# Kernel tuning notes

Hardware: AMD Instinct MI355X
Metric: run time of the kernel (lower is better)

## Reference

```python
import jax, jax.numpy as jnp
import numpy as np
import math

B, S, HID = 2, 2048, 4096
NH, NKV, HD = 32, 8, 128
ROPE_BASE = 10000.0


def _rope_tables(b, s, hd):
    inv_freq = 1.0 / (ROPE_BASE ** (jnp.arange(0, hd, 2, dtype=jnp.float32) / hd))
    t = jnp.arange(s, dtype=jnp.float32)
    freqs = jnp.outer(t, inv_freq)            # [s, hd/2]
    emb = jnp.concatenate([freqs, freqs], -1)  # [s, hd]
    cos = jnp.broadcast_to(jnp.cos(emb)[None], (b, s, hd))
    sin = jnp.broadcast_to(jnp.sin(emb)[None], (b, s, hd))
    return cos, sin


def setup_inputs() -> dict:
    key = jax.random.key(0)
    ks = jax.random.split(key, 5)
    hidden_states = jax.random.normal(ks[0], (B, S, HID), dtype=jnp.float32)
    # additive causal mask [B,1,S,S]: 0 on/below diagonal, large negative above
    causal = jnp.tril(jnp.ones((S, S), dtype=bool))
    attention_mask = jnp.where(causal, 0.0, jnp.finfo(jnp.float32).min)[None, None]
    attention_mask = jnp.broadcast_to(attention_mask, (B, 1, S, S)).astype(jnp.float32)
    cos, sin = _rope_tables(B, S, HD)
    sc = 0.02
    Wq = jax.random.normal(ks[1], (NH * HD, HID), dtype=jnp.float32) * sc
    Wk = jax.random.normal(ks[2], (NKV * HD, HID), dtype=jnp.float32) * sc
    Wv = jax.random.normal(ks[3], (NKV * HD, HID), dtype=jnp.float32) * sc
    Wo = jax.random.normal(ks[4], (HID, NH * HD), dtype=jnp.float32) * sc
    return {"hidden_states": hidden_states, "attention_mask": attention_mask,
            "cos": cos, "sin": sin, "Wq": Wq, "Wk": Wk, "Wv": Wv, "Wo": Wo}


def _rotate_half(x):
    x1, x2 = jnp.split(x, 2, axis=-1)
    return jnp.concatenate([-x2, x1], axis=-1)


def reference(hidden_states, attention_mask, cos, sin, Wq, Wk, Wv, Wo):
    b, s, _ = hidden_states.shape
    # projections (nn.Linear: x @ W.T, no bias)
    q = jnp.einsum('bsh,oh->bso', hidden_states, Wq).reshape(b, s, NH, HD).transpose(0, 2, 1, 3)
    k = jnp.einsum('bsh,oh->bso', hidden_states, Wk).reshape(b, s, NKV, HD).transpose(0, 2, 1, 3)
    v = jnp.einsum('bsh,oh->bso', hidden_states, Wv).reshape(b, s, NKV, HD).transpose(0, 2, 1, 3)
    # RoPE (cos/sin: [b,s,hd] -> unsqueeze head dim)
    c, sn = cos[:, None], sin[:, None]
    q = q * c + _rotate_half(q) * sn
    k = k * c + _rotate_half(k) * sn
    # repeat_kv: [b,nkv,s,d] -> [b,nh,s,d] (repeat_interleave over head dim)
    n_rep = NH // NKV
    k = jnp.repeat(k, n_rep, axis=1)
    v = jnp.repeat(v, n_rep, axis=1)
    # eager attention
    scores = jnp.einsum('bhqd,bhkd->bhqk', q, k) / math.sqrt(HD)
    scores = scores + attention_mask[:, :, :, :k.shape[2]]
    probs = jax.nn.softmax(scores.astype(jnp.float32), axis=-1).astype(q.dtype)
    attn = jnp.einsum('bhqk,bhkd->bhqd', probs, v)
    attn = attn.transpose(0, 2, 1, 3).reshape(b, s, NH * HD)
    return jnp.einsum('bso,ho->bsh', attn, Wo)
```

## Files before the change

### kernel.cpp

```cpp
#include <hip/hip_runtime.h>
#include <hip/hip_bf16.h>
#include <cstdint>

#define S_LEN 2048
#define HIDDEN 4096
#define NH 32
#define NKV 8
#define HD 128
#define BATCH 2
#define MROWS (BATCH * S_LEN)

typedef float f32x4 __attribute__((ext_vector_type(4)));
typedef __bf16 bf16x8 __attribute__((ext_vector_type(8)));
typedef __bf16 bf16x4 __attribute__((ext_vector_type(4)));

static __device__ inline f32x4 mfma16(bf16x8 a, bf16x8 b, f32x4 c) {
    return __builtin_amdgcn_mfma_f32_16x16x32_bf16(a, b, c, 0, 0, 0);
}

static __device__ inline void gl_lds16(const __bf16* g, __bf16* l) {
    __builtin_amdgcn_global_load_lds(
        (const __attribute__((address_space(1))) void*)g,
        (__attribute__((address_space(3))) void*)l, 16, 0, 0);
}

#define LGKM0()  asm volatile("s_waitcnt lgkmcnt(0)" ::: "memory")
#define SCHEDB() __builtin_amdgcn_sched_barrier(0)
#define SBAR()   __builtin_amdgcn_s_barrier()

__global__ __launch_bounds__(256) void conv_f32_bf16(const float* __restrict__ in,
                                                     __bf16* __restrict__ out, int n8) {
    int i = blockIdx.x * 256 + threadIdx.x;
    if (i >= n8) return;
    const float4* p = (const float4*)in + (size_t)i * 2;
    float4 a = p[0], b = p[1];
    bf16x8 v;
    v[0] = (__bf16)a.x; v[1] = (__bf16)a.y; v[2] = (__bf16)a.z; v[3] = (__bf16)a.w;
    v[4] = (__bf16)b.x; v[5] = (__bf16)b.y; v[6] = (__bf16)b.z; v[7] = (__bf16)b.w;
    ((bf16x8*)out)[i] = v;
}

template<int MODE, int BM>
__global__ __launch_bounds__(512, 2) void gemm256(const __bf16* __restrict__ A,
                                                  const __bf16* __restrict__ B,
                                                  float* __restrict__ Cf,
                                                  __bf16* __restrict__ Qo,
                                                  __bf16* __restrict__ Ko,
                                                  __bf16* __restrict__ Vo,
                                                  int N, int K, int nbx) {
    constexpr int MF = BM / 32;
    constexpr int MH = BM / 64;
    __shared__ __bf16 As[2][BM * 64];
    __shared__ __bf16 Bs[2][256 * 64];
    const int tid = threadIdx.x, lane = tid & 63;
    const int lq = lane & 15, hi2 = lane >> 4;
    const int wv = tid >> 6;
    const int wr = wv >> 2, wc = wv & 3;

    const int cpx = gridDim.x >> 3;
    const int bid = blockIdx.x;
    const int swz = (bid & 7) * cpx + (bid >> 3);
    const int bx = swz % nbx, by = swz / nbx;
    const int brow = by * BM, bcol = bx * 256;

    f32x4 acc[MF][4] = {};
    bf16x8 af[MH][2], bfr[2][2];
    const int NT = K >> 6;

    auto stageA = [&](int bb, int kt, int roff) {
        #pragma unroll
        for (int r = 0; r < 2; ++r) {
            int i = r * 512 + tid;
            int row = i >> 3, sl = i & 7, lsl = sl ^ (row & 7);
            gl_lds16(A + (size_t)(brow + roff + row) * K + kt * 64 + lsl * 8,
                     &As[bb][roff * 64 + i * 8]);
        }
    };
    auto stageB = [&](int bb, int kt, int roff) {
        #pragma unroll
        for (int r = 0; r < 2; ++r) {
            int i = r * 512 + tid;
            int row = i >> 3, sl = i & 7, lsl = sl ^ (row & 7);
            gl_lds16(B + (size_t)(bcol + roff + row) * K + kt * 64 + lsl * 8,
                     &Bs[bb][roff * 64 + i * 8]);
        }
    };
    auto loadA = [&](int bb, int mq) {
        #pragma unroll
        for (int mi = 0; mi < MH; ++mi) {
            int row = wr * (BM / 2) + (mq * MH + mi) * 16 + lq;
            #pragma unroll
            for (int kk = 0; kk < 2; ++kk) {
                int lsl = (kk * 4 + hi2) ^ (row & 7);
                af[mi][kk] = *(const bf16x8*)&As[bb][row * 64 + lsl * 8];
            }
        }
    };
    auto loadB = [&](int bb, int nq) {
        #pragma unroll
        for (int ni = 0; ni < 2; ++ni) {
            int row = wc * 64 + (nq * 2 + ni) * 16 + lq;
            #pragma unroll
            for (int kk = 0; kk < 2; ++kk) {
                int lsl = (kk * 4 + hi2) ^ (row & 7);
                bfr[ni][kk] = *(const bf16x8*)&Bs[bb][row * 64 + lsl * 8];
            }
        }
    };
    auto mmaq = [&](int mq, int nq) {
        __builtin_amdgcn_s_setprio(1);
        #pragma unroll
        for (int kk = 0; kk < 2; ++kk)
            #pragma unroll
            for (int mi = 0; mi < MH; ++mi)
                #pragma unroll
                for (int ni = 0; ni < 2; ++ni)
                    acc[mq * MH + mi][nq * 2 + ni] =
                        mfma16(af[mi][kk], bfr[ni][kk], acc[mq * MH + mi][nq * 2 + ni]);
        __builtin_amdgcn_s_setprio(0);
    };

    stageA(0, 0, 0);
    if constexpr (BM == 256) stageA(0, 0, 128);
    stageB(0, 0, 0);
    stageB(0, 0, 128);

    for (int t = 0; t < NT; ++t) {
        const int cur = t & 1, nxt = cur ^ 1;
        const int tn = (t + 1 < NT) ? t + 1 : NT - 1;
        stageA(nxt, tn, 0);
        if constexpr (BM == 256) stageA(nxt, tn, 128);
        stageB(nxt, tn, 0);
        if constexpr (BM == 256) { asm volatile("s_waitcnt vmcnt(6)" ::: "memory"); }
        else                     { asm volatile("s_waitcnt vmcnt(4)" ::: "memory"); }
        SBAR(); SCHEDB();
        loadA(cur, 0); loadB(cur, 0);
        LGKM0(); SCHEDB();
        mmaq(0, 0);
        SBAR(); SCHEDB();
        loadB(cur, 1);
        stageB(nxt, tn, 128);
        SBAR(); SCHEDB();
        LGKM0(); SCHEDB();
        mmaq(0, 1);
        SBAR(); SCHEDB();
        loadA(cur, 1);
        SBAR(); SCHEDB();
        LGKM0(); SCHEDB();
        mmaq(1, 1);
        SBAR(); SCHEDB();
        loadB(cur, 0);
        SBAR(); SCHEDB();
        LGKM0(); SCHEDB();
        mmaq(1, 0);
        SBAR(); SCHEDB();
    }

    #pragma unroll
    for (int m = 0; m < MF; ++m) {
        #pragma unroll
        for (int n = 0; n < 4; ++n) {
            int row0 = brow + wr * (BM / 2) + m * 16 + (hi2 << 2);
            int col  = bcol + wc * 64 + n * 16 + lq;
            if constexpr (MODE == 3) {
                if (col < NKV * HD) {
                    #pragma unroll
                    for (int j = 0; j < 4; ++j)
                        Ko[(size_t)(row0 + j) * (NKV * HD) + col] = (__bf16)acc[m][n][j];
                } else {
                    int c2 = col - NKV * HD;
                    int hkv = c2 >> 7, d = c2 & (HD - 1);
                    int bb2 = row0 >> 11, s = row0 & (S_LEN - 1);
                    bf16x4 t4;
                    #pragma unroll
                    for (int j = 0; j < 4; ++j) t4[j] = (__bf16)acc[m][n][j];
                    *(bf16x4*)&Vo[((size_t)((bb2 * NKV + hkv) * HD + d)) * S_LEN + s] = t4;
                }
            } else if constexpr (MODE == 1) {
                #pragma unroll
                for (int j = 0; j < 4; ++j)
                    Cf[(size_t)(row0 + j) * N + col] = acc[m][n][j];
            } else {
                #pragma unroll
                for (int j = 0; j < 4; ++j)
                    Qo[(size_t)(row0 + j) * N + col] = (__bf16)acc[m][n][j];
            }
        }
    }
}

__global__ __launch_bounds__(256) void rope_kernel(__bf16* __restrict__ X,
                                                   const float* __restrict__ ct,
                                                   const float* __restrict__ st,
                                                   int nheads, int total) {
    int idx = blockIdx.x * 256 + threadIdx.x;
    if (idx >= total) return;
    int d  = idx & 63;
    int hh = (idx >> 6) % nheads;
    int m  = idx / (64 * nheads);
    __bf16* p = X + (size_t)m * (nheads * HD) + hh * HD;
    float c = ct[(size_t)m * HD + d];
    float s = st[(size_t)m * HD + d];
    float x1 = (float)p[d], x2 = (float)p[d + 64];
    p[d]      = (__bf16)(x1 * c - x2 * s);
    p[d + 64] = (__bf16)(x2 * c + x1 * s);
}

__global__ __launch_bounds__(256, 3) void attn_kernel(const __bf16* __restrict__ Q,
                                                      const __bf16* __restrict__ K,
                                                      const __bf16* __restrict__ V,
                                                      __bf16* __restrict__ O) {
    constexpr int QB = 128, KB = 32;
    constexpr int nqb = S_LEN / QB;
    const int bid = blockIdx.x;
    const int qb  = nqb - 1 - (bid % nqb);
    const int h   = (bid / nqb) % NH;
    const int b   = bid / (nqb * NH);
    const int hkv = h >> 2;
    const int tid = threadIdx.x, lane = tid & 63, w = tid >> 6;
    const int lq = lane & 15, hi2 = lane >> 4;
    const int q0 = qb * QB, qrow_lo = q0 + w * 32;

    __shared__ __bf16 Ks[2][KB * HD];
    __shared__ __bf16 Vt[2][HD * KB];
    __shared__ __bf16 Pl[4][2][16][40];

    bf16x8 qf[2][4];
    #pragma unroll
    for (int mt = 0; mt < 2; ++mt) {
        int row = qrow_lo + mt * 16 + lq;
        const __bf16* qp = Q + ((size_t)(b * S_LEN + row)) * (NH * HD) + h * HD + hi2 * 8;
        #pragma unroll
        for (int c = 0; c < 4; ++c) qf[mt][c] = *(const bf16x8*)(qp + c * 32);
    }

    f32x4 o_acc[2][8] = {};
    float m_r[2] = {-1e30f, -1e30f}, l_r[2] = {0.f, 0.f};
    const float scale = 0.08838834764831843f;
    const int nkb = (q0 + QB) / KB;

    auto stage = [&](int bb, int k0s) {
        #pragma unroll
        for (int r = 0; r < 2; ++r) {
            int i = r * 256 + tid;
            {   int row = i >> 4, sl = i & 15, lsl = sl ^ (row & 7);
                gl_lds16(&K[((size_t)(b * S_LEN + k0s + row)) * (NKV * HD) + hkv * HD + lsl * 8],
                         &Ks[bb][i * 8]); }
            {   int d = i >> 2, sl = i & 3, lsl = sl ^ (d & 3);
                gl_lds16(&V[((size_t)((b * NKV + hkv) * HD + d)) * S_LEN + k0s + lsl * 8],
                         &Vt[bb][i * 8]); }
        }
    };

    stage(0, 0);
    for (int kb = 0; kb < nkb; ++kb) {
        int kn = (kb + 1 < nkb) ? kb + 1 : kb;
        stage((kb + 1) & 1, kn * KB);
        asm volatile("s_waitcnt vmcnt(4)" ::: "memory");
        SBAR(); SCHEDB();
        const int cur = kb & 1;
        const int k0  = kb * KB;
        const __bf16* ks = &Ks[cur][0];
        const __bf16* vt = &Vt[cur][0];

        f32x4 sc[2][2] = {};
        #pragma unroll
        for (int t = 0; t < 2; ++t) {
            int krow = t * 16 + lq;
            #pragma unroll
            for (int c = 0; c < 4; ++c) {
                int psl = (c * 4 + hi2) ^ (krow & 7);
                bf16x8 kf = *(const bf16x8*)&ks[krow * HD + psl * 8];
                sc[0][t] = mfma16(kf, qf[0][c], sc[0][t]);
                sc[1][t] = mfma16(kf, qf[1][c], sc[1][t]);
            }
        }

        #pragma unroll
        for (int mt = 0; mt < 2; ++mt) {
            int q_abs = qrow_lo + mt * 16 + lq;
            #pragma unroll
            for (int t = 0; t < 2; ++t)
                #pragma unroll
                for (int j = 0; j < 4; ++j) {
                    int kv_abs = k0 + t * 16 + hi2 * 4 + j;
                    sc[mt][t][j] = (kv_abs > q_abs) ? -1e30f : sc[mt][t][j] * scale;
                }
            float pmax = fmaxf(
                fmaxf(fmaxf(sc[mt][0][0], sc[mt][0][1]), fmaxf(sc[mt][0][2], sc[mt][0][3])),
                fmaxf(fmaxf(sc[mt][1][0], sc[mt][1][1]), fmaxf(sc[mt][1][2], sc[mt][1][3])));
            pmax = fmaxf(pmax, __shfl_xor(pmax, 16));
            pmax = fmaxf(pmax, __shfl_xor(pmax, 32));
            float mn = fmaxf(m_r[mt], pmax);
            float sf = __expf(m_r[mt] - mn);
            m_r[mt] = mn;
            float rs = 0.f;
            #pragma unroll
            for (int t = 0; t < 2; ++t)
                #pragma unroll
                for (int j = 0; j < 4; ++j) {
                    float p = __expf(sc[mt][t][j] - mn);
                    sc[mt][t][j] = p;
                    rs += p;
                }
            rs += __shfl_xor(rs, 16);
            rs += __shfl_xor(rs, 32);
            l_r[mt] = l_r[mt] * sf + rs;
            #pragma unroll
            for (int dt = 0; dt < 8; ++dt)
                #pragma unroll
                for (int j = 0; j < 4; ++j) o_acc[mt][dt][j] *= sf;
            #pragma unroll
            for (int t = 0; t < 2; ++t) {
                bf16x4 pw;
                #pragma unroll
                for (int j = 0; j < 4; ++j) pw[j] = (__bf16)sc[mt][t][j];
                *(bf16x4*)&Pl[w][mt][lq][t * 16 + hi2 * 4] = pw;
            }
        }

        LGKM0(); SCHEDB();
        bf16x8 pf0 = *(const bf16x8*)&Pl[w][0][lq][hi2 * 8];
        bf16x8 pf1 = *(const bf16x8*)&Pl[w][1][lq][hi2 * 8];

        #pragma unroll
        for (int dt = 0; dt < 8; ++dt) {
            int vrow = dt * 16 + lq;
            int psl  = hi2 ^ (vrow & 3);
            bf16x8 vf = *(const bf16x8*)&vt[vrow * KB + psl * 8];
            o_acc[0][dt] = mfma16(vf, pf0, o_acc[0][dt]);
            o_acc[1][dt] = mfma16(vf, pf1, o_acc[1][dt]);
        }
        LGKM0(); SCHEDB();
        SBAR(); SCHEDB();
    }

    #pragma unroll
    for (int mt = 0; mt < 2; ++mt) {
        float inv = 1.0f / l_r[mt];
        int q_abs = qrow_lo + mt * 16 + lq;
        __bf16* op = O + ((size_t)(b * S_LEN + q_abs)) * (NH * HD) + h * HD;
        #pragma unroll
        for (int dt = 0; dt < 8; ++dt) {
            bf16x4 t4;
            #pragma unroll
            for (int j = 0; j < 4; ++j) t4[j] = (__bf16)(o_acc[mt][dt][j] * inv);
            *(bf16x4*)&op[dt * 16 + hi2 * 4] = t4;
        }
    }
}

extern "C" void kernel_launch(void* const* d_in, const int* in_sizes, int n_in,
                              void* d_out, int out_size, void* d_ws, size_t ws_size,
                              hipStream_t stream) {
    const float* X  = (const float*)d_in[0];
    const float* ct = (const float*)d_in[2];
    const float* st = (const float*)d_in[3];
    const float* Wq = (const float*)d_in[4];
    const float* Wk = (const float*)d_in[5];
    const float* Wv = (const float*)d_in[6];
    const float* Wo = (const float*)d_in[7];
    float* out = (float*)d_out;

    const size_t MEL  = (size_t)MROWS * HIDDEN;
    const size_t KVEL = (size_t)MROWS * (NKV * HD);
    const int NQKV = NH * HD + 2 * NKV * HD;

    __bf16* Wqkv = (__bf16*)d_ws;
    __bf16* Xb   = Wqkv + (size_t)NQKV * HIDDEN;
    __bf16* Qb   = Xb + MEL;
    __bf16* Kb   = Qb + MEL;
    __bf16* VtG  = Kb + KVEL;
    __bf16* Ab   = Wqkv;
    __bf16* Wob  = Xb;

    dim3 blk(256);
    hipLaunchKernelGGL(conv_f32_bf16, dim3((int)(MEL / 8 / 256)), blk, 0, stream, X,  Xb, (int)(MEL / 8));
    hipLaunchKernelGGL(conv_f32_bf16, dim3((int)(MEL / 8 / 256)), blk, 0, stream, Wq, Wqkv, (int)(MEL / 8));
    hipLaunchKernelGGL(conv_f32_bf16, dim3((int)(KVEL / 8 / 256)), blk, 0, stream,
                       Wk, Wqkv + (size_t)HIDDEN * HIDDEN, (int)(KVEL / 8));
    hipLaunchKernelGGL(conv_f32_bf16, dim3((int)(KVEL / 8 / 256)), blk, 0, stream,
                       Wv, Wqkv + (size_t)(HIDDEN + NKV * HD) * HIDDEN, (int)(KVEL / 8));

    hipLaunchKernelGGL((gemm256<0, 256>), dim3(256), dim3(512), 0, stream,
                       Xb, Wqkv, nullptr, Qb, nullptr, nullptr, NH * HD, HIDDEN, 16);
    hipLaunchKernelGGL((gemm256<3, 128>), dim3(256), dim3(512), 0, stream,
                       Xb, Wqkv + (size_t)HIDDEN * HIDDEN, nullptr, nullptr, Kb, VtG,
                       2 * NKV * HD, HIDDEN, 8);

    hipLaunchKernelGGL(rope_kernel, dim3((MROWS * NH * 64) / 256), blk, 0, stream,
                       Qb, ct, st, NH, MROWS * NH * 64);
    hipLaunchKernelGGL(rope_kernel, dim3((MROWS * NKV * 64) / 256), blk, 0, stream,
                       Kb, ct, st, NKV, MROWS * NKV * 64);

    hipLaunchKernelGGL(conv_f32_bf16, dim3((int)(MEL / 8 / 256)), blk, 0, stream, Wo, Wob, (int)(MEL / 8));

    hipLaunchKernelGGL(attn_kernel, dim3(BATCH * NH * (S_LEN / 128)), blk, 0, stream,
                       Qb, Kb, VtG, Ab);

    hipLaunchKernelGGL((gemm256<1, 256>), dim3(256), dim3(512), 0, stream,
                       Ab, Wob, out, nullptr, nullptr, nullptr, HIDDEN, HIDDEN, 16);
}
```

Baseline: 675.9 us.

## Pair causal query blocks per workgroup and use lazy exp2 softmax rescaling

Each attention workgroup now processes two complementary query blocks (a long one and a short one), so all 512 workgroups do equal causal work. The grid is remapped to spread workgroups across XCDs. The K/V prefetch pipeline runs continuously across both passes. Separately, the softmax scale and log2(e) are folded into Q, exp is replaced by exp2, masking runs only on diagonal tiles, and rescaling of the accumulator is skipped unless the running max grows by more than a threshold. Risks are higher register pressure from the loop nesting and slightly different numerics from folding the scale into bf16 Q.

```diff
diff --git a/kernel.cpp b/kernel.cpp
--- a/kernel.cpp
+++ b/kernel.cpp
@@ -212,32 +212,23 @@
                                                       __bf16* __restrict__ O) {
     constexpr int QB = 128, KB = 32;
     constexpr int nqb = S_LEN / QB;
-    const int bid = blockIdx.x;
-    const int qb  = nqb - 1 - (bid % nqb);
-    const int h   = (bid / nqb) % NH;
-    const int b   = bid / (nqb * NH);
+    const int cpx = gridDim.x >> 3;
+    const int b0 = blockIdx.x;
+    const int bid = (b0 & 7) * cpx + (b0 >> 3);
+    const int pair = bid & 7;
+    const int h    = (bid >> 3) & (NH - 1);
+    const int b    = bid >> 8;
     const int hkv = h >> 2;
     const int tid = threadIdx.x, lane = tid & 63, w = tid >> 6;
     const int lq = lane & 15, hi2 = lane >> 4;
-    const int q0 = qb * QB, qrow_lo = q0 + w * 32;
 
     __shared__ __bf16 Ks[2][KB * HD];
     __shared__ __bf16 Vt[2][HD * KB];
     __shared__ __bf16 Pl[4][2][16][40];
 
-    bf16x8 qf[2][4];
-    #pragma unroll
-    for (int mt = 0; mt < 2; ++mt) {
-        int row = qrow_lo + mt * 16 + lq;
-        const __bf16* qp = Q + ((size_t)(b * S_LEN + row)) * (NH * HD) + h * HD + hi2 * 8;
-        #pragma unroll
-        for (int c = 0; c < 4; ++c) qf[mt][c] = *(const bf16x8*)(qp + c * 32);
-    }
-
-    f32x4 o_acc[2][8] = {};
-    float m_r[2] = {-1e30f, -1e30f}, l_r[2] = {0.f, 0.f};
-    const float scale = 0.08838834764831843f;
-    const int nkb = (q0 + QB) / KB;
+    const int qbA = nqb - 1 - pair;
+    const int nkbA = 4 * (qbA + 1);
+    const int T = nkbA + 4 * (pair + 1);
 
     auto stage = [&](int bb, int k0s) {
         #pragma unroll
@@ -252,100 +243,134 @@
         }
     };
 
+    const float c2 = 0.08838834764831843f * 1.4426950408889634f;
+
     stage(0, 0);
-    for (int kb = 0; kb < nkb; ++kb) {
-        int kn = (kb + 1 < nkb) ? kb + 1 : kb;
-        stage((kb + 1) & 1, kn * KB);
-        asm volatile("s_waitcnt vmcnt(4)" ::: "memory");
-        SBAR(); SCHEDB();
-        const int cur = kb & 1;
-        const int k0  = kb * KB;
-        const __bf16* ks = &Ks[cur][0];
-        const __bf16* vt = &Vt[cur][0];
-
-        f32x4 sc[2][2] = {};
-        #pragma unroll
-        for (int t = 0; t < 2; ++t) {
-            int krow = t * 16 + lq;
+    int tt = 0;
+    #pragma unroll 1
+    for (int pass = 0; pass < 2; ++pass) {
+        const int qb = pass ? pair : qbA;
+        const int q0 = qb * QB, qrow_lo = q0 + w * 32;
+        const int nkb = 4 * (qb + 1);
+
+        bf16x8 qf[2][4];
+        #pragma unroll
+        for (int mt = 0; mt < 2; ++mt) {
+            int row = qrow_lo + mt * 16 + lq;
+            const __bf16* qp = Q + ((size_t)(b * S_LEN + row)) * (NH * HD) + h * HD + hi2 * 8;
             #pragma unroll
             for (int c = 0; c < 4; ++c) {
-                int psl = (c * 4 + hi2) ^ (krow & 7);
-                bf16x8 kf = *(const bf16x8*)&ks[krow * HD + psl * 8];
-                sc[0][t] = mfma16(kf, qf[0][c], sc[0][t]);
-                sc[1][t] = mfma16(kf, qf[1][c], sc[1][t]);
-            }
+                bf16x8 v = *(const bf16x8*)(qp + c * 32);
+                #pragma unroll
+                for (int e = 0; e < 8; ++e) v[e] = (__bf16)((float)v[e] * c2);
+                qf[mt][c] = v;
+            }
+        }
+
+        f32x4 o_acc[2][8] = {};
+        float m_r[2] = {-1e30f, -1e30f}, l_r[2] = {0.f, 0.f};
+
+        #pragma unroll 1
+        for (int kb = 0; kb < nkb; ++kb, ++tt) {
+            int tn = (tt + 1 < T) ? tt + 1 : T - 1;
+            int k0n = (tn < nkbA ? tn : tn - nkbA) * KB;
+            stage((tt + 1) & 1, k0n);
+            asm volatile("s_waitcnt vmcnt(4)" ::: "memory");
+            SBAR(); SCHEDB();
+            const int cur = tt & 1;
+            const int k0  = kb * KB;
+            const __bf16* ks = &Ks[cur][0];
+            const __bf16* vt = &Vt[cur][0];
+
+            f32x4 sc[2][2] = {};
+            #pragma unroll
+            for (int t = 0; t < 2; ++t) {
+                int krow = t * 16 + lq;
+                #pragma unroll
+                for (int c = 0; c < 4; ++c) {
+                    int psl = (c * 4 + hi2) ^ (krow & 7);
+                    bf16x8 kf = *(const bf16x8*)&ks[krow * HD + psl * 8];
+                    sc[0][t] = mfma16(kf, qf[0][c], sc[0][t]);
+                    sc[1][t] = mfma16(kf, qf[1][c], sc[1][t]);
+                }
+            }
+
+            #pragma unroll
+            for (int mt = 0; mt < 2; ++mt) {
+                int q_abs = qrow_lo + mt * 16 + lq;
+                if (k0 + KB - 1 > qrow_lo + mt * 16) {
+                    #pragma unroll
+                    for (int t = 0; t < 2; ++t)
+                        #pragma unroll
+                        for (int j = 0; j < 4; ++j) {
+                            int kv_abs = k0 + t * 16 + hi2 * 4 + j;
+                            if (kv_abs > q_abs) sc[mt][t][j] = -1e30f;
+                        }
+                }
+                float pmax = fmaxf(
+                    fmaxf(fmaxf(sc[mt][0][0], sc[mt][0][1]), fmaxf(sc[mt][0][2], sc[mt][0][3])),
+                    fmaxf(fmaxf(sc[mt][1][0], sc[mt][1][1]), fmaxf(sc[mt][1][2], sc[mt][1][3])));
+                pmax = fmaxf(pmax, __shfl_xor(pmax, 16));
+                pmax = fmaxf(pmax, __shfl_xor(pmax, 32));
+                if (!__all(pmax - m_r[mt] <= 8.0f)) {
+                    float mn = fmaxf(m_r[mt], pmax);
+                    float sf = __builtin_amdgcn_exp2f(m_r[mt] - mn);
+                    m_r[mt] = mn;
+                    l_r[mt] *= sf;
+                    #pragma unroll
+                    for (int dt = 0; dt < 8; ++dt)
+                        #pragma unroll
+                        for (int j = 0; j < 4; ++j) o_acc[mt][dt][j] *= sf;
+                }
+                float rs = 0.f;
+                #pragma unroll
+                for (int t = 0; t < 2; ++t)
+                    #pragma unroll
+                    for (int j = 0; j < 4; ++j) {
+                        float p = __builtin_amdgcn_exp2f(sc[mt][t][j] - m_r[mt]);
+                        sc[mt][t][j] = p;
+                        rs += p;
+                    }
+                rs += __shfl_xor(rs, 16);
+                rs += __shfl_xor(rs, 32);
+                l_r[mt] += rs;
+                #pragma unroll
+                for (int t = 0; t < 2; ++t) {
+                    bf16x4 pw;
+                    #pragma unroll
+                    for (int j = 0; j < 4; ++j) pw[j] = (__bf16)sc[mt][t][j];
+                    *(bf16x4*)&Pl[w][mt][lq][t * 16 + hi2 * 4] = pw;
+                }
+            }
+
+            LGKM0(); SCHEDB();
+            bf16x8 pf0 = *(const bf16x8*)&Pl[w][0][lq][hi2 * 8];
+            bf16x8 pf1 = *(const bf16x8*)&Pl[w][1][lq][hi2 * 8];
+
+            #pragma unroll
+            for (int dt = 0; dt < 8; ++dt) {
+                int vrow = dt * 16 + lq;
+                int psl  = hi2 ^ (vrow & 3);
+                bf16x8 vf = *(const bf16x8*)&vt[vrow * KB + psl * 8];
+                o_acc[0][dt] = mfma16(vf, pf0, o_acc[0][dt]);
+                o_acc[1][dt] = mfma16(vf, pf1, o_acc[1][dt]);
+            }
+            LGKM0(); SCHEDB();
+            SBAR(); SCHEDB();
         }
 
         #pragma unroll
         for (int mt = 0; mt < 2; ++mt) {
+            float inv = 1.0f / l_r[mt];
             int q_abs = qrow_lo + mt * 16 + lq;
-            #pragma unroll
-            for (int t = 0; t < 2; ++t)
-                #pragma unroll
-                for (int j = 0; j < 4; ++j) {
-                    int kv_abs = k0 + t * 16 + hi2 * 4 + j;
-                    sc[mt][t][j] = (kv_abs > q_abs) ? -1e30f : sc[mt][t][j] * scale;
-                }
-            float pmax = fmaxf(
-                fmaxf(fmaxf(sc[mt][0][0], sc[mt][0][1]), fmaxf(sc[mt][0][2], sc[mt][0][3])),
-                fmaxf(fmaxf(sc[mt][1][0], sc[mt][1][1]), fmaxf(sc[mt][1][2], sc[mt][1][3])));
-            pmax = fmaxf(pmax, __shfl_xor(pmax, 16));
-            pmax = fmaxf(pmax, __shfl_xor(pmax, 32));
-            float mn = fmaxf(m_r[mt], pmax);
-            float sf = __expf(m_r[mt] - mn);
-            m_r[mt] = mn;
-            float rs = 0.f;
-            #pragma unroll
-            for (int t = 0; t < 2; ++t)
-                #pragma unroll
-                for (int j = 0; j < 4; ++j) {
-                    float p = __expf(sc[mt][t][j] - mn);
-                    sc[mt][t][j] = p;
-                    rs += p;
-                }
-            rs += __shfl_xor(rs, 16);
-            rs += __shfl_xor(rs, 32);
-            l_r[mt] = l_r[mt] * sf + rs;
-            #pragma unroll
-            for (int dt = 0; dt < 8; ++dt)
-                #pragma unroll
-                for (int j = 0; j < 4; ++j) o_acc[mt][dt][j] *= sf;
-            #pragma unroll
-            for (int t = 0; t < 2; ++t) {
-                bf16x4 pw;
-                #pragma unroll
-                for (int j = 0; j < 4; ++j) pw[j] = (__bf16)sc[mt][t][j];
-                *(bf16x4*)&Pl[w][mt][lq][t * 16 + hi2 * 4] = pw;
-            }
-        }
-
-        LGKM0(); SCHEDB();
-        bf16x8 pf0 = *(const bf16x8*)&Pl[w][0][lq][hi2 * 8];
-        bf16x8 pf1 = *(const bf16x8*)&Pl[w][1][lq][hi2 * 8];
-
-        #pragma unroll
-        for (int dt = 0; dt < 8; ++dt) {
-            int vrow = dt * 16 + lq;
-            int psl  = hi2 ^ (vrow & 3);
-            bf16x8 vf = *(const bf16x8*)&vt[vrow * KB + psl * 8];
-            o_acc[0][dt] = mfma16(vf, pf0, o_acc[0][dt]);
-            o_acc[1][dt] = mfma16(vf, pf1, o_acc[1][dt]);
-        }
-        LGKM0(); SCHEDB();
-        SBAR(); SCHEDB();
-    }
-
-    #pragma unroll
-    for (int mt = 0; mt < 2; ++mt) {
-        float inv = 1.0f / l_r[mt];
-        int q_abs = qrow_lo + mt * 16 + lq;
-        __bf16* op = O + ((size_t)(b * S_LEN + q_abs)) * (NH * HD) + h * HD;
-        #pragma unroll
-        for (int dt = 0; dt < 8; ++dt) {
-            bf16x4 t4;
-            #pragma unroll
-            for (int j = 0; j < 4; ++j) t4[j] = (__bf16)(o_acc[mt][dt][j] * inv);
-            *(bf16x4*)&op[dt * 16 + hi2 * 4] = t4;
+            __bf16* op = O + ((size_t)(b * S_LEN + q_abs)) * (NH * HD) + h * HD;
+            #pragma unroll
+            for (int dt = 0; dt < 8; ++dt) {
+                bf16x4 t4;
+                #pragma unroll
+                for (int j = 0; j < 4; ++j) t4[j] = (__bf16)(o_acc[mt][dt][j] * inv);
+                *(bf16x4*)&op[dt * 16 + hi2 * 4] = t4;
+            }
         }
     }
 }
@@ -395,8 +420,7 @@
 
     hipLaunchKernelGGL(conv_f32_bf16, dim3((int)(MEL / 8 / 256)), blk, 0, stream, Wo, Wob, (int)(MEL / 8));
 
-    hipLaunchKernelGGL(attn_kernel, dim3(BATCH * NH * (S_LEN / 128)), blk, 0, stream,
-                       Qb, Kb, VtG, Ab);
+    hipLaunchKernelGGL(attn_kernel, dim3(512), blk, 0, stream, Qb, Kb, VtG, Ab);
 
     hipLaunchKernelGGL((gemm256<1, 256>), dim3(256), dim3(512), 0, stream,
                        Ab, Wob, out, nullptr, nullptr, nullptr, HIDDEN, HIDDEN, 16);
```

New measurement: 586.6 us. -13.2%, faster.
